# Kernel tuning notes

Measured on AMD Instinct MI355X. Metric: run time of the kernel, lower is better.

Reference implementation:

```python
import jax, jax.numpy as jnp
import numpy as np

B, C, H, W = 8, 256, 64, 64
C8 = C // 8


def setup_inputs() -> dict:
    key = jax.random.key(0)
    ks = jax.random.split(key, 8)
    x = jax.random.normal(ks[0], (B, C, H, W), dtype=jnp.float32)
    # 1x1 convs == channel matmuls; store as [out_ch, in_ch] plus bias
    Wq = jax.random.normal(ks[1], (C8, C), dtype=jnp.float32) * (1.0 / np.sqrt(C))
    bq = jnp.zeros((C8,), dtype=jnp.float32)
    Wk = jax.random.normal(ks[2], (C8, C), dtype=jnp.float32) * (1.0 / np.sqrt(C))
    bk = jnp.zeros((C8,), dtype=jnp.float32)
    Wv = jax.random.normal(ks[3], (C, C), dtype=jnp.float32) * (1.0 / np.sqrt(C))
    bv = jnp.zeros((C,), dtype=jnp.float32)
    # gamma initialized to zero in the module, but use a nonzero value so the
    # attention branch actually contributes to the output being checked
    gamma = jnp.full((1,), 0.5, dtype=jnp.float32)
    return {"x": x, "Wq": Wq, "bq": bq, "Wk": Wk, "bk": bk, "Wv": Wv, "bv": bv, "gamma": gamma}


def reference(x, Wq, bq, Wk, bk, Wv, bv, gamma):
    b, c, h, w = x.shape
    n = h * w
    xf = x.reshape(b, c, n)                                  # [B, C, N]
    q = jnp.einsum('oc,bcn->bon', Wq, xf) + bq[None, :, None]  # [B, C8, N]
    k = jnp.einsum('oc,bcn->bon', Wk, xf) + bk[None, :, None]  # [B, C8, N]
    v = jnp.einsum('oc,bcn->bon', Wv, xf) + bv[None, :, None]  # [B, C,  N]
    # attention[b, i, j] = sum_d q[b, d, i] * k[b, d, j]  (no 1/sqrt(d) scaling!)
    scores = jnp.einsum('bdi,bdj->bij', q, k)                # [B, N, N]
    attn = jax.nn.softmax(scores, axis=-1)                   # softmax over j
    # out[b, c, i] = sum_j v[b, c, j] * attn[b, i, j]
    out = jnp.einsum('bcj,bij->bci', v, attn)                # [B, C, N]
    out = out.reshape(b, c, h, w)
    return gamma[0] * out + x
```

## Files before the change

kernel.cpp:

```cpp
#include <hip/hip_runtime.h>
#include <math.h>

#define BB 8
#define CC 256
#define NN 4096

typedef float f4 __attribute__((ext_vector_type(4)));
typedef short bh8 __attribute__((ext_vector_type(8)));

__device__ __forceinline__ unsigned short f2bf(float f) {
    unsigned u = __builtin_bit_cast(unsigned, f);
    u += 0x7fff + ((u >> 16) & 1);
    return (unsigned short)(u >> 16);
}
__device__ __forceinline__ unsigned packbf(float a, float b) {
    return (unsigned)f2bf(a) | ((unsigned)f2bf(b) << 16);
}

__device__ __forceinline__ float exp2_fast(float x) {
    float r;
    asm("v_exp_f32 %0, %1" : "=v"(r) : "v"(x));
    return r;
}

__global__ void prep_w_kernel(const float* __restrict__ Wq, const float* __restrict__ bq,
                              const float* __restrict__ Wk, const float* __restrict__ bk,
                              const float* __restrict__ Wv, const float* __restrict__ bv,
                              unsigned short* __restrict__ Whi, unsigned short* __restrict__ Wlo,
                              float* __restrict__ bcat) {
    const float L2E = 1.4426950408889634f;
    int idx = blockIdx.x * 256 + threadIdx.x;
    if (idx < 320) {
        bcat[idx] = (idx < 32) ? bq[idx] * L2E : (idx < 64 ? bk[idx - 32] : bv[idx - 64]);
    }
    if (idx < 320 * 256) {
        int o = idx >> 8;
        int c = idx & 255;
        float v = (o < 32) ? Wq[o * 256 + c] * L2E
                           : (o < 64 ? Wk[(o - 32) * 256 + c] : Wv[(o - 64) * 256 + c]);
        unsigned short hi = f2bf(v);
        float vhi = __builtin_bit_cast(float, ((unsigned)hi) << 16);
        Whi[idx] = hi;
        Wlo[idx] = f2bf(v - vhi);
    }
}

__global__ __launch_bounds__(256, 2) void qkv_kernel(
    const float* __restrict__ x, const unsigned short* __restrict__ Whi,
    const unsigned short* __restrict__ Wlo, const float* __restrict__ bcat,
    unsigned short* __restrict__ q64, unsigned short* __restrict__ k64,
    unsigned short* __restrict__ vC) {
    __shared__ __align__(16) char smem[67584];
    unsigned short* xsTh = (unsigned short*)smem;
    unsigned short* xsTl = (unsigned short*)(smem + 33792);
    unsigned short* qkl = (unsigned short*)smem;
    unsigned short* vsl = (unsigned short*)(smem + 16384);

    int blk = blockIdx.x;
    int b = blk >> 6;
    int i0 = (blk & 63) << 6;
    int t = threadIdx.x;
    const float* xb = x + ((size_t)b << 20);

    for (int idx = t; idx < 256 * 64; idx += 256) {
        int c = idx >> 6, ii = idx & 63;
        float v = xb[((size_t)c << 12) + i0 + ii];
        unsigned short hi = f2bf(v);
        float vhi = __builtin_bit_cast(float, ((unsigned)hi) << 16);
        xsTh[ii * 264 + c] = hi;
        xsTl[ii * 264 + c] = f2bf(v - vhi);
    }
    __syncthreads();

    int lane = t & 63;
    int w = t >> 6;
    int g = lane >> 4;
    int li = lane & 15;

    f4 acc[5][4];
#pragma unroll
    for (int tt = 0; tt < 5; ++tt)
#pragma unroll
        for (int it = 0; it < 4; ++it) acc[tt][it] = (f4){0.f, 0.f, 0.f, 0.f};

#pragma unroll
    for (int tt = 0; tt < 5; ++tt) {
        int ot = w + 4 * tt;
        bool qk = (ot < 4);
        const unsigned short* wrh = Whi + (size_t)(16 * ot + li) * 256 + 8 * g;
        const unsigned short* wrl = Wlo + (size_t)(16 * ot + li) * 256 + 8 * g;
        bh8 ah[8], al[8];
#pragma unroll
        for (int ck = 0; ck < 8; ++ck) {
            ah[ck] = *(const bh8*)(wrh + 32 * ck);
            al[ck] = *(const bh8*)(wrl + 32 * ck);
        }
#pragma unroll
        for (int it = 0; it < 4; ++it) {
            const unsigned short* xrh = xsTh + (16 * it + li) * 264 + 8 * g;
            const unsigned short* xrl = xsTl + (16 * it + li) * 264 + 8 * g;
            f4 a = acc[tt][it];
            if (qk) {
#pragma unroll
                for (int ck = 0; ck < 8; ++ck) {
                    bh8 xh = *(const bh8*)(xrh + 32 * ck);
                    bh8 xl = *(const bh8*)(xrl + 32 * ck);
                    a = __builtin_amdgcn_mfma_f32_16x16x32_bf16(ah[ck], xh, a, 0, 0, 0);
                    a = __builtin_amdgcn_mfma_f32_16x16x32_bf16(al[ck], xh, a, 0, 0, 0);
                    a = __builtin_amdgcn_mfma_f32_16x16x32_bf16(ah[ck], xl, a, 0, 0, 0);
                }
            } else {
#pragma unroll
                for (int ck = 0; ck < 8; ++ck) {
                    bh8 xh = *(const bh8*)(xrh + 32 * ck);
                    a = __builtin_amdgcn_mfma_f32_16x16x32_bf16(ah[ck], xh, a, 0, 0, 0);
                    a = __builtin_amdgcn_mfma_f32_16x16x32_bf16(al[ck], xh, a, 0, 0, 0);
                }
            }
            acc[tt][it] = a;
        }
    }
    __syncthreads();

#pragma unroll
    for (int tt = 0; tt < 5; ++tt) {
        int ot = w + 4 * tt;
        float bias[4];
#pragma unroll
        for (int e = 0; e < 4; ++e) bias[e] = bcat[16 * ot + 4 * g + e];
#pragma unroll
        for (int it = 0; it < 4; ++it) {
            int ii = 16 * it + li;
#pragma unroll
            for (int e = 0; e < 4; ++e) {
                int o = 16 * ot + 4 * g + e;
                float v = acc[tt][it][e] + bias[e];
                if (o < 64) {
                    unsigned short hi = f2bf(v);
                    float vhi = __builtin_bit_cast(float, ((unsigned)hi) << 16);
                    unsigned short lo = f2bf(v - vhi);
                    if (o < 32) {
                        qkl[ii * 128 + o] = hi;
                        qkl[ii * 128 + 32 + o] = lo;
                    } else {
                        qkl[ii * 128 + 32 + o] = hi;
                        qkl[ii * 128 + 64 + o] = lo;
                    }
                } else {
                    vsl[(o - 64) * 66 + ii] = f2bf(v);
                }
            }
        }
    }
    __syncthreads();

    const unsigned* qk32 = (const unsigned*)qkl;
    unsigned* qb = (unsigned*)(q64 + ((size_t)(b * NN + i0)) * 64);
    unsigned* kb = (unsigned*)(k64 + ((size_t)(b * NN + i0)) * 64);
    for (int idx = t; idx < 64 * 32; idx += 256) {
        int row = idx >> 5, dw = idx & 31;
        qb[row * 32 + dw] = qk32[row * 64 + dw];
        kb[row * 32 + dw] = qk32[row * 64 + 32 + dw];
    }
    for (int idx = t; idx < 256 * 32; idx += 256) {
        int c = idx >> 5, dw = idx & 31;
        unsigned val = *(const unsigned*)(vsl + c * 66 + 2 * dw);
        int i = 2 * dw;
        int p = 32 * (i >> 5) + 8 * ((i >> 2) & 3) + 4 * ((i >> 4) & 1) + (i & 3);
        *(unsigned*)(vC + ((size_t)(b * CC + c)) * NN + i0 + p) = val;
    }
}

__global__ __launch_bounds__(256, 2) void attn_kernel(
    const unsigned short* __restrict__ q64, const unsigned short* __restrict__ k64,
    const unsigned short* __restrict__ vC, const float* __restrict__ x,
    const float* __restrict__ gamma, float* __restrict__ out) {
    __shared__ unsigned short vs[2][256 * 64];

    int t = threadIdx.x;
    int lane = t & 63;
    int w = t >> 6;
    int g = lane >> 4;
    int li = lane & 15;
    int blk = blockIdx.x;
    int b = blk & 7;
    int i0 = (blk >> 3) << 6;
    int qb = i0 + 16 * w;

    const unsigned short* vb = vC + ((size_t)b * CC) * NN;
    const unsigned short* kb = k64 + ((size_t)b * NN) * 64;

    bh8 qf[2];
#pragma unroll
    for (int s = 0; s < 2; ++s)
        qf[s] = *(const bh8*)(q64 + ((size_t)(b * NN + qb + li)) * 64 + s * 32 + 8 * g);

    const unsigned short* vsrcb[8];
#pragma unroll
    for (int s = 0; s < 8; ++s) {
        int c = 64 * w + 8 * s + (lane >> 3);
        int slot = (lane & 7) ^ (c & 7);
        vsrcb[s] = vb + (size_t)c * NN + slot * 8;
    }
    const unsigned short* ksrcb[8];
#pragma unroll
    for (int jt = 0; jt < 4; ++jt)
#pragma unroll
        for (int s = 0; s < 2; ++s)
            ksrcb[jt * 2 + s] = kb + (size_t)(16 * jt + li) * 64 + s * 32 + 8 * g;

    f4 acc[16];
#pragma unroll
    for (int ct = 0; ct < 16; ++ct) acc[ct] = (f4){0.f, 0.f, 0.f, 0.f};
    float m, l;

    auto stageV = [&](int buf, int j0) {
#pragma unroll
        for (int s = 0; s < 8; ++s) {
            __builtin_amdgcn_global_load_lds(
                (const __attribute__((address_space(1))) unsigned int*)(vsrcb[s] + j0),
                (__attribute__((address_space(3))) unsigned int*)(&vs[buf][(64 * w + 8 * s) * 64]),
                16, 0, 0);
        }
    };
    auto loadK = [&](bh8 (&kf)[4][2], int j0) {
        size_t joff = (size_t)j0 * 64;
#pragma unroll
        for (int jt = 0; jt < 4; ++jt)
#pragma unroll
            for (int s = 0; s < 2; ++s)
                kf[jt][s] = *(const bh8*)(ksrcb[jt * 2 + s] + joff);
    };
    auto qkComp = [&](f4 (&sOut)[4], bh8 (&kc)[4][2]) {
#pragma unroll
        for (int jt = 0; jt < 4; ++jt) {
            f4 a = {0.f, 0.f, 0.f, 0.f};
            a = __builtin_amdgcn_mfma_f32_16x16x32_bf16(kc[jt][0], qf[0], a, 0, 0, 0);
            a = __builtin_amdgcn_mfma_f32_16x16x32_bf16(kc[jt][1], qf[0], a, 0, 0, 0);
            a = __builtin_amdgcn_mfma_f32_16x16x32_bf16(kc[jt][0], qf[1], a, 0, 0, 0);
            sOut[jt] = a;
        }
    };
    auto packP = [&](f4 (&sT)[4], bh8 (&pN)[2]) {
        union { unsigned u[4]; bh8 v; } pf0, pf1;
        pf0.u[0] = packbf(sT[0][0], sT[0][1]);
        pf0.u[1] = packbf(sT[0][2], sT[0][3]);
        pf0.u[2] = packbf(sT[1][0], sT[1][1]);
        pf0.u[3] = packbf(sT[1][2], sT[1][3]);
        pf1.u[0] = packbf(sT[2][0], sT[2][1]);
        pf1.u[1] = packbf(sT[2][2], sT[2][3]);
        pf1.u[2] = packbf(sT[3][0], sT[3][1]);
        pf1.u[3] = packbf(sT[3][2], sT[3][3]);
        pN[0] = pf0.v;
        pN[1] = pf1.v;
    };

    bh8 kf0[4][2], kf1[4][2];
    bh8 P0[2], P1[2];

    stageV(0, 0);
    loadK(kf0, 0);
    loadK(kf1, 64);
    {
        f4 sT[4];
        qkComp(sT, kf0);
        float mx = sT[0][0];
#pragma unroll
        for (int jt = 0; jt < 4; ++jt)
#pragma unroll
            for (int e = 0; e < 4; ++e) mx = fmaxf(mx, sT[jt][e]);
        mx = fmaxf(mx, __shfl_xor(mx, 16));
        mx = fmaxf(mx, __shfl_xor(mx, 32));
        m = mx;
        float sum = 0.f;
#pragma unroll
        for (int jt = 0; jt < 4; ++jt)
#pragma unroll
            for (int e = 0; e < 4; ++e) {
                float p = exp2_fast(sT[jt][e] - m);
                sT[jt][e] = p;
                sum += p;
            }
        l = sum;
        packP(sT, P0);
    }
    __syncthreads();

    auto step = [&](int tt, bh8 (&kNext)[4][2], bh8 (&kLoad)[4][2],
                    bh8 (&pC)[2], bh8 (&pN)[2], int buf) {
        if (tt < 63) stageV(buf ^ 1, (tt + 1) << 6);
        if (tt < 62) loadK(kLoad, (tt + 2) << 6);

        bool resc = false;
        float sc = 1.f;
        if (tt < 63) {
            f4 sT[4];
            qkComp(sT, kNext);
            float mx = sT[0][0];
#pragma unroll
            for (int jt = 0; jt < 4; ++jt)
#pragma unroll
                for (int e = 0; e < 4; ++e) mx = fmaxf(mx, sT[jt][e]);
            if (!__all(mx <= m + 11.541561f)) {
                mx = fmaxf(mx, __shfl_xor(mx, 16));
                mx = fmaxf(mx, __shfl_xor(mx, 32));
                float mnew = fmaxf(m, mx);
                sc = exp2_fast(m - mnew);
                l *= sc;
                m = mnew;
                resc = true;
            }
            float sum = 0.f;
#pragma unroll
            for (int jt = 0; jt < 4; ++jt)
#pragma unroll
                for (int e = 0; e < 4; ++e) {
                    float p = exp2_fast(sT[jt][e] - m);
                    sT[jt][e] = p;
                    sum += p;
                }
            l += sum;
            packP(sT, pN);
        }

        const char* vsb = (const char*)vs[buf];
        auto vld = [&](int ct, int h) -> bh8 {
            int off = (16 * ct + li) * 128 + ((64 * h + 16 * g) ^ ((li & 7) << 4));
            return *(const bh8*)(vsb + off);
        };
        bh8 va[8], vb2[8];
#pragma unroll
        for (int ct = 0; ct < 8; ++ct) va[ct] = vld(ct, 0);
#pragma unroll
        for (int ct = 0; ct < 8; ++ct) vb2[ct] = vld(ct + 8, 0);
#pragma unroll
        for (int ct = 0; ct < 8; ++ct)
            acc[ct] = __builtin_amdgcn_mfma_f32_16x16x32_bf16(va[ct], pC[0], acc[ct], 0, 0, 0);
#pragma unroll
        for (int ct = 0; ct < 8; ++ct) va[ct] = vld(ct, 1);
#pragma unroll
        for (int ct = 0; ct < 8; ++ct)
            acc[ct + 8] = __builtin_amdgcn_mfma_f32_16x16x32_bf16(vb2[ct], pC[0], acc[ct + 8], 0, 0, 0);
#pragma unroll
        for (int ct = 0; ct < 8; ++ct) vb2[ct] = vld(ct + 8, 1);
#pragma unroll
        for (int ct = 0; ct < 8; ++ct)
            acc[ct] = __builtin_amdgcn_mfma_f32_16x16x32_bf16(va[ct], pC[1], acc[ct], 0, 0, 0);
#pragma unroll
        for (int ct = 0; ct < 8; ++ct)
            acc[ct + 8] = __builtin_amdgcn_mfma_f32_16x16x32_bf16(vb2[ct], pC[1], acc[ct + 8], 0, 0, 0);

        if (resc) {
#pragma unroll
            for (int ct = 0; ct < 16; ++ct)
#pragma unroll
                for (int e = 0; e < 4; ++e) acc[ct][e] *= sc;
        }
        __syncthreads();
    };

    for (int tt = 0; tt < 64; tt += 2) {
        step(tt, kf1, kf0, P0, P1, 0);
        step(tt + 1, kf0, kf1, P1, P0, 1);
    }

    l += __shfl_xor(l, 16);
    l += __shfl_xor(l, 32);

    float gm = gamma[0];
    float rl = 1.f / l;
    const float* xb = x + ((size_t)b * CC) * NN;
    float* ob = out + ((size_t)b * CC) * NN;
    int i = qb + li;
#pragma unroll
    for (int ct = 0; ct < 16; ++ct)
#pragma unroll
        for (int e = 0; e < 4; ++e) {
            int c = 16 * ct + 4 * g + e;
            size_t idx = (size_t)c * NN + i;
            ob[idx] = gm * (acc[ct][e] * rl) + xb[idx];
        }
}

extern "C" void kernel_launch(void* const* d_in, const int* in_sizes, int n_in,
                              void* d_out, int out_size, void* d_ws, size_t ws_size,
                              hipStream_t stream) {
    const float* x = (const float*)d_in[0];
    const float* Wq = (const float*)d_in[1];
    const float* bq = (const float*)d_in[2];
    const float* Wk = (const float*)d_in[3];
    const float* bk = (const float*)d_in[4];
    const float* Wv = (const float*)d_in[5];
    const float* bv = (const float*)d_in[6];
    const float* gamma = (const float*)d_in[7];
    float* out = (float*)d_out;

    unsigned short* ws16 = (unsigned short*)d_ws;
    unsigned short* q64w = ws16;
    unsigned short* k64w = ws16 + 2097152;
    unsigned short* vCw = ws16 + 4194304;
    unsigned short* Whiw = ws16 + 12582912;
    unsigned short* Wlow = Whiw + 81920;
    float* bcatw = (float*)(Wlow + 81920);

    prep_w_kernel<<<320, 256, 0, stream>>>(Wq, bq, Wk, bk, Wv, bv, Whiw, Wlow, bcatw);
    qkv_kernel<<<BB * (NN / 64), 256, 0, stream>>>(x, Whiw, Wlow, bcatw, q64w, k64w, vCw);
    attn_kernel<<<512, 256, 0, stream>>>(q64w, k64w, vCw, x, gamma, out);
}
```

Before: 205.7 us.

## Store V in MFMA fragment layout and load directly from global, dropping LDS staging

The qkv kernel now writes V in a per-lane fragment-ordered layout so each lane's MFMA operand is a single contiguous 16-byte load. The attention kernel removes the LDS double buffer and global_load_lds staging for V, reading fragments directly from global memory each step. Block barriers are reduced to once every eight steps. This removes LDS traffic and synchronisation, but each wave now fetches the whole V tile separately and the loads are not prefetched, exposing global latency and raising L2 traffic.

```diff
diff --git a/kernel.cpp b/kernel.cpp
--- a/kernel.cpp
+++ b/kernel.cpp
@@ -49,7 +49,7 @@
     const float* __restrict__ x, const unsigned short* __restrict__ Whi,
     const unsigned short* __restrict__ Wlo, const float* __restrict__ bcat,
     unsigned short* __restrict__ q64, unsigned short* __restrict__ k64,
-    unsigned short* __restrict__ vC) {
+    unsigned short* __restrict__ vF) {
     __shared__ __align__(16) char smem[67584];
     unsigned short* xsTh = (unsigned short*)smem;
     unsigned short* xsTl = (unsigned short*)(smem + 33792);
@@ -162,21 +162,26 @@
         qb[row * 32 + dw] = qk32[row * 64 + dw];
         kb[row * 32 + dw] = qk32[row * 64 + 32 + dw];
     }
-    for (int idx = t; idx < 256 * 32; idx += 256) {
-        int c = idx >> 5, dw = idx & 31;
-        unsigned val = *(const unsigned*)(vsl + c * 66 + 2 * dw);
-        int i = 2 * dw;
-        int p = 32 * (i >> 5) + 8 * ((i >> 2) & 3) + 4 * ((i >> 4) & 1) + (i & 3);
-        *(unsigned*)(vC + ((size_t)(b * CC + c)) * NN + i0 + p) = val;
+    {
+        unsigned short* vFb = vF + (((size_t)b * 64 + (i0 >> 6)) * 32) * 512;
+#pragma unroll
+        for (int it = 0; it < 8; ++it) {
+            int f = it * 4 + w;
+            int ct = f >> 1, h = f & 1;
+            const unsigned short* src =
+                vsl + (16 * ct + li) * 66 + 32 * h + 8 * (g >> 1) + 4 * (g & 1);
+            union { unsigned short s[8]; uint4 u; } tmp;
+#pragma unroll
+            for (int e = 0; e < 8; ++e) tmp.s[e] = src[16 * (e >> 2) + (e & 3)];
+            *(uint4*)(vFb + ((size_t)f * 64 + lane) * 8) = tmp.u;
+        }
     }
 }
 
 __global__ __launch_bounds__(256, 2) void attn_kernel(
     const unsigned short* __restrict__ q64, const unsigned short* __restrict__ k64,
-    const unsigned short* __restrict__ vC, const float* __restrict__ x,
+    const unsigned short* __restrict__ vF, const float* __restrict__ x,
     const float* __restrict__ gamma, float* __restrict__ out) {
-    __shared__ unsigned short vs[2][256 * 64];
-
     int t = threadIdx.x;
     int lane = t & 63;
     int w = t >> 6;
@@ -187,7 +192,7 @@
     int i0 = (blk >> 3) << 6;
     int qb = i0 + 16 * w;
 
-    const unsigned short* vb = vC + ((size_t)b * CC) * NN;
+    const unsigned short* vFb = vF + (size_t)b * (64 * 32 * 512) + lane * 8;
     const unsigned short* kb = k64 + ((size_t)b * NN) * 64;
 
     bh8 qf[2];
@@ -195,13 +200,6 @@
     for (int s = 0; s < 2; ++s)
         qf[s] = *(const bh8*)(q64 + ((size_t)(b * NN + qb + li)) * 64 + s * 32 + 8 * g);
 
-    const unsigned short* vsrcb[8];
-#pragma unroll
-    for (int s = 0; s < 8; ++s) {
-        int c = 64 * w + 8 * s + (lane >> 3);
-        int slot = (lane & 7) ^ (c & 7);
-        vsrcb[s] = vb + (size_t)c * NN + slot * 8;
-    }
     const unsigned short* ksrcb[8];
 #pragma unroll
     for (int jt = 0; jt < 4; ++jt)
@@ -214,15 +212,6 @@
     for (int ct = 0; ct < 16; ++ct) acc[ct] = (f4){0.f, 0.f, 0.f, 0.f};
     float m, l;
 
-    auto stageV = [&](int buf, int j0) {
-#pragma unroll
-        for (int s = 0; s < 8; ++s) {
-            __builtin_amdgcn_global_load_lds(
-                (const __attribute__((address_space(1))) unsigned int*)(vsrcb[s] + j0),
-                (__attribute__((address_space(3))) unsigned int*)(&vs[buf][(64 * w + 8 * s) * 64]),
-                16, 0, 0);
-        }
-    };
     auto loadK = [&](bh8 (&kf)[4][2], int j0) {
         size_t joff = (size_t)j0 * 64;
 #pragma unroll
@@ -230,6 +219,9 @@
 #pragma unroll
             for (int s = 0; s < 2; ++s)
                 kf[jt][s] = *(const bh8*)(ksrcb[jt * 2 + s] + joff);
+    };
+    auto vload = [&](int f, int tt) -> bh8 {
+        return *(const bh8*)(vFb + ((size_t)tt * 32 + f) * 512);
     };
     auto qkComp = [&](f4 (&sOut)[4], bh8 (&kc)[4][2]) {
 #pragma unroll
@@ -258,7 +250,6 @@
     bh8 kf0[4][2], kf1[4][2];
     bh8 P0[2], P1[2];
 
-    stageV(0, 0);
     loadK(kf0, 0);
     loadK(kf1, 64);
     {
@@ -284,11 +275,9 @@
         l = sum;
         packP(sT, P0);
     }
-    __syncthreads();
 
     auto step = [&](int tt, bh8 (&kNext)[4][2], bh8 (&kLoad)[4][2],
-                    bh8 (&pC)[2], bh8 (&pN)[2], int buf) {
-        if (tt < 63) stageV(buf ^ 1, (tt + 1) << 6);
+                    bh8 (&pC)[2], bh8 (&pN)[2]) {
         if (tt < 62) loadK(kLoad, (tt + 2) << 6);
 
         bool resc = false;
@@ -323,26 +312,21 @@
             packP(sT, pN);
         }
 
-        const char* vsb = (const char*)vs[buf];
-        auto vld = [&](int ct, int h) -> bh8 {
-            int off = (16 * ct + li) * 128 + ((64 * h + 16 * g) ^ ((li & 7) << 4));
-            return *(const bh8*)(vsb + off);
-        };
         bh8 va[8], vb2[8];
 #pragma unroll
-        for (int ct = 0; ct < 8; ++ct) va[ct] = vld(ct, 0);
-#pragma unroll
-        for (int ct = 0; ct < 8; ++ct) vb2[ct] = vld(ct + 8, 0);
+        for (int ct = 0; ct < 8; ++ct) va[ct] = vload(2 * ct, tt);
+#pragma unroll
+        for (int ct = 0; ct < 8; ++ct) vb2[ct] = vload(2 * (ct + 8), tt);
 #pragma unroll
         for (int ct = 0; ct < 8; ++ct)
             acc[ct] = __builtin_amdgcn_mfma_f32_16x16x32_bf16(va[ct], pC[0], acc[ct], 0, 0, 0);
 #pragma unroll
-        for (int ct = 0; ct < 8; ++ct) va[ct] = vld(ct, 1);
+        for (int ct = 0; ct < 8; ++ct) va[ct] = vload(2 * ct + 1, tt);
 #pragma unroll
         for (int ct = 0; ct < 8; ++ct)
             acc[ct + 8] = __builtin_amdgcn_mfma_f32_16x16x32_bf16(vb2[ct], pC[0], acc[ct + 8], 0, 0, 0);
 #pragma unroll
-        for (int ct = 0; ct < 8; ++ct) vb2[ct] = vld(ct + 8, 1);
+        for (int ct = 0; ct < 8; ++ct) vb2[ct] = vload(2 * (ct + 8) + 1, tt);
 #pragma unroll
         for (int ct = 0; ct < 8; ++ct)
             acc[ct] = __builtin_amdgcn_mfma_f32_16x16x32_bf16(va[ct], pC[1], acc[ct], 0, 0, 0);
@@ -356,12 +340,12 @@
 #pragma unroll
                 for (int e = 0; e < 4; ++e) acc[ct][e] *= sc;
         }
-        __syncthreads();
+        if ((tt & 7) == 7) __syncthreads();
     };
 
     for (int tt = 0; tt < 64; tt += 2) {
-        step(tt, kf1, kf0, P0, P1, 0);
-        step(tt + 1, kf0, kf1, P1, P0, 1);
+        step(tt, kf1, kf0, P0, P1);
+        step(tt + 1, kf0, kf1, P1, P0);
     }
 
     l += __shfl_xor(l, 16);
@@ -398,12 +382,12 @@
     unsigned short* ws16 = (unsigned short*)d_ws;
     unsigned short* q64w = ws16;
     unsigned short* k64w = ws16 + 2097152;
-    unsigned short* vCw = ws16 + 4194304;
+    unsigned short* vFw = ws16 + 4194304;
     unsigned short* Whiw = ws16 + 12582912;
     unsigned short* Wlow = Whiw + 81920;
     float* bcatw = (float*)(Wlow + 81920);
 
     prep_w_kernel<<<320, 256, 0, stream>>>(Wq, bq, Wk, bk, Wv, bv, Whiw, Wlow, bcatw);
-    qkv_kernel<<<BB * (NN / 64), 256, 0, stream>>>(x, Whiw, Wlow, bcatw, q64w, k64w, vCw);
-    attn_kernel<<<512, 256, 0, stream>>>(q64w, k64w, vCw, x, gamma, out);
-}
+    qkv_kernel<<<BB * (NN / 64), 256, 0, stream>>>(x, Whiw, Wlow, bcatw, q64w, k64w, vFw);
+    attn_kernel<<<512, 256, 0, stream>>>(q64w, k64w, vFw, x, gamma, out);
+}
```

Result: slower. 317.7 us (+54.4%).
